# Kernel optimization log

Measured on AMD Instinct MI355X. Metric: run time of the kernel, lower is better.

Reference implementation:

```python
import jax, jax.numpy as jnp
import numpy as np

N_NODES = 10000
N_EDGES = 160000
N_GRAPHS = 64
X_IN = 128
HID = 64
EDGE_DIM = 16
HEADS = 4
# (in_dim, out_dim_per_head) for the 3 TransformerConv layers (concat=False)
DIMS = [(X_IN, HID), (HID, 2 * HID), (2 * HID, HID)]
WNAMES = [f"{n}{l}" for l in (1, 2, 3) for n in ("wq", "bq", "wk", "bk", "wv", "bv", "we", "ws", "bs")]


def setup_inputs() -> dict:
    key = jax.random.key(0)
    ks = iter(jax.random.split(key, 64))
    inp = {}
    inp["x"] = jax.random.normal(next(ks), (N_NODES, X_IN), jnp.float32)
    inp["edge_index"] = jax.random.randint(next(ks), (2, N_EDGES), 0, N_NODES)
    inp["edge_attr"] = jax.random.normal(next(ks), (N_EDGES, EDGE_DIM), jnp.float32)
    inp["batch"] = jnp.sort(jax.random.randint(next(ks), (N_NODES,), 0, N_GRAPHS))
    for l, (din, dout) in enumerate(DIMS, 1):
        hd = HEADS * dout
        for nm, shape in [("wq", (din, hd)), ("wk", (din, hd)), ("wv", (din, hd)),
                          ("we", (EDGE_DIM, hd)), ("ws", (din, dout))]:
            inp[f"{nm}{l}"] = jax.random.normal(next(ks), shape, jnp.float32) * 0.05
        inp[f"bq{l}"] = jnp.zeros((hd,), jnp.float32)
        inp[f"bk{l}"] = jnp.zeros((hd,), jnp.float32)
        inp[f"bv{l}"] = jnp.zeros((hd,), jnp.float32)
        inp[f"bs{l}"] = jnp.zeros((dout,), jnp.float32)
    return inp


def _transformer_conv(x, src, dst, edge_attr, wq, bq, wk, bk, wv, bv, we, ws, bs, dout):
    """PyG TransformerConv, concat=False, root_weight=True, with edge features."""
    N = x.shape[0]
    q = (x @ wq + bq).reshape(N, HEADS, dout)
    k = (x @ wk + bk).reshape(N, HEADS, dout)
    v = (x @ wv + bv).reshape(N, HEADS, dout)
    e = (edge_attr @ we).reshape(-1, HEADS, dout)  # [E, H, C]
    k_j = k[src] + e                               # edge-conditioned keys
    alpha = jnp.einsum("ehd,ehd->eh", q[dst], k_j) * (1.0 / float(dout) ** 0.5)  # [E, H]
    # numerically stable segment softmax over incoming edges of each dst node
    a_max = jax.ops.segment_max(alpha, dst, num_segments=N)
    ex = jnp.exp(alpha - a_max[dst])
    den = jax.ops.segment_sum(ex, dst, num_segments=N)
    attn = ex / den[dst]
    agg = jax.ops.segment_sum((v[src] + e) * attn[..., None], dst, num_segments=N)  # [N, H, C]
    return agg.mean(axis=1) + x @ ws + bs  # concat=False -> head mean; + skip


def _forward(x, edge_attr, edge_index, batch, params):
    src, dst = edge_index[0], edge_index[1]
    h = x
    for l, (_, dout) in enumerate(DIMS, 1):
        p = [params[f"{n}{l}"] for n in ("wq", "bq", "wk", "bk", "wv", "bv", "we", "ws", "bs")]
        h = jax.nn.elu(_transformer_conv(h, src, dst, edge_attr, *p, dout))
    # global mean pool over graphs
    s = jax.ops.segment_sum(h, batch, num_segments=N_GRAPHS)
    cnt = jax.ops.segment_sum(jnp.ones((h.shape[0], 1), h.dtype), batch, num_segments=N_GRAPHS)
    return s / jnp.maximum(cnt, 1.0)


def reference(x, edge_index, edge_attr, batch,
              wq1, bq1, wk1, bk1, wv1, bv1, we1, ws1, bs1,
              wq2, bq2, wk2, bk2, wv2, bv2, we2, ws2, bs2,
              wq3, bq3, wk3, bk3, wv3, bv3, we3, ws3, bs3):
    params = dict(locals())
    return _forward(x, edge_attr, edge_index, batch, params)
```

## Files before the change

kernel.cpp:

```cpp
#include <hip/hip_runtime.h>
#include <hip/hip_fp16.h>
#include <math.h>

#define N_NODES 10000
#define N_EDGES 160000
#define N_GRAPHS 64

using half8 = __attribute__((ext_vector_type(8))) _Float16;
using floatx4 = __attribute__((ext_vector_type(4))) float;

template <int NV> struct KW;
template <> struct KW<1> { using T = uint2; };
template <> struct KW<2> { using T = uint4; };

__device__ inline void cvt_kv(const uint2& w, float4* dst) {
  float2 a = __half22float2(*reinterpret_cast<const __half2*>(&w.x));
  float2 b = __half22float2(*reinterpret_cast<const __half2*>(&w.y));
  dst[0] = make_float4(a.x, a.y, b.x, b.y);
}
__device__ inline void cvt_kv(const uint4& w, float4* dst) {
  float2 a = __half22float2(*reinterpret_cast<const __half2*>(&w.x));
  float2 b = __half22float2(*reinterpret_cast<const __half2*>(&w.y));
  float2 c = __half22float2(*reinterpret_cast<const __half2*>(&w.z));
  float2 d = __half22float2(*reinterpret_cast<const __half2*>(&w.w));
  dst[0] = make_float4(a.x, a.y, b.x, b.y);
  dst[1] = make_float4(c.x, c.y, d.x, d.y);
}

template <int K, int HD, int DOUT>
__global__ __launch_bounds__(256) void gemm_mfma(
    const __half* __restrict__ A, const __half* __restrict__ Wp,
    const float* __restrict__ bias, __half* __restrict__ QS,
    __half* __restrict__ KV, int M) {
  constexpr int QSS = HD + 64 + DOUT;
  constexpr int KS = K / 32;
  const int tid = threadIdx.x;
  const int wave = tid >> 6, lane = tid & 63;
  const int quad = lane >> 4, n16 = lane & 15;
  const int row0 = blockIdx.y * 64 + wave * 16;
  const int col0 = blockIdx.x * 64;
  const int nblk0 = blockIdx.x * 4;

  const int arow = min(row0 + n16, M - 1);
  half8 afrag[KS];
#pragma unroll
  for (int s = 0; s < KS; ++s)
    afrag[s] = *reinterpret_cast<const half8*>(A + (size_t)arow * K + s * 32 + quad * 8);

  floatx4 acc[4];
#pragma unroll
  for (int t = 0; t < 4; ++t) {
    acc[t] = (floatx4){0.f, 0.f, 0.f, 0.f};
#pragma unroll
    for (int s = 0; s < KS; ++s) {
      half8 bf = *reinterpret_cast<const half8*>(
          Wp + (((size_t)(nblk0 + t) * KS + s) * 64 + lane) * 8);
      acc[t] = __builtin_amdgcn_mfma_f32_16x16x32_f16(afrag[s], bf, acc[t], 0, 0, 0);
    }
  }

#pragma unroll
  for (int t = 0; t < 4; ++t) {
    const int c = col0 + t * 16 + n16;
    const float bv = bias[c];
#pragma unroll
    for (int r = 0; r < 4; ++r) {
      int row = row0 + quad * 4 + r;
      if (row < M) {
        __half val = __float2half(acc[t][r] + bv);
        if (c < HD + 64)
          QS[(size_t)row * QSS + c] = val;
        else if (c < 3 * HD + 64)
          KV[(size_t)row * (2 * HD) + (c - HD - 64)] = val;
        else
          QS[(size_t)row * QSS + HD + 64 + (c - 3 * HD - 64)] = val;
      }
    }
  }
}

__device__ inline void pack_layer(int i, int K, int HD, int DOUT, float scale,
                                  const float* wq, const float* wk,
                                  const float* wv, const float* wsk,
                                  const float* we, const float* bq,
                                  const float* bk, const float* bv,
                                  const float* bs, __half* Wp, float* bcat) {
  const int W = 3 * HD + DOUT + 64;
  const int KS = K / 32;
  if (i < K * W) {
    int j = i & 7, lane = (i >> 3) & 63, fs = i >> 9;
    int nblk = fs / KS, s = fs - nblk * KS;
    int quad = lane >> 4, n = lane & 15;
    int k = s * 32 + quad * 8 + j, c = nblk * 16 + n;
    float v;
    if (c < HD) {
      v = wq[k * HD + c] * scale;
    } else if (c < HD + 64) {
      int gi = c - HD, hh = gi >> 4, d = gi & 15;
      float a = 0.f;
      for (int cc = 0; cc < DOUT; ++cc)
        a += wq[k * HD + hh * DOUT + cc] * we[d * HD + hh * DOUT + cc];
      v = a * scale;
    } else if (c < 2 * HD + 64) {
      v = wk[k * HD + (c - HD - 64)];
    } else if (c < 3 * HD + 64) {
      v = wv[k * HD + (c - 2 * HD - 64)];
    } else {
      v = wsk[k * DOUT + (c - 3 * HD - 64)];
    }
    Wp[i] = __float2half(v);
  } else {
    int c = i - K * W;
    float v;
    if (c < HD) {
      v = bq[c] * scale;
    } else if (c < HD + 64) {
      int gi = c - HD, hh = gi >> 4, d = gi & 15;
      float a = 0.f;
      for (int cc = 0; cc < DOUT; ++cc)
        a += bq[hh * DOUT + cc] * we[d * HD + hh * DOUT + cc];
      v = a * scale;
    } else if (c < 2 * HD + 64) {
      v = bk[c - HD - 64];
    } else if (c < 3 * HD + 64) {
      v = bv[c - 2 * HD - 64];
    } else {
      v = bs[c - 3 * HD - 64];
    }
    bcat[c] = v;
  }
}

#define T1 115584
#define T2 227904
#define T3 343488
#define TCONV (N_NODES * 32)
#define TTOT (T3 + TCONV)

__global__ void pack_all(
    const float* wq1, const float* wk1, const float* wv1, const float* ws1,
    const float* we1, const float* bq1, const float* bk1, const float* bv1,
    const float* bs1,
    const float* wq2, const float* wk2, const float* wv2, const float* ws2,
    const float* we2, const float* bq2, const float* bk2, const float* bv2,
    const float* bs2,
    const float* wq3, const float* wk3, const float* wv3, const float* ws3,
    const float* we3, const float* bq3, const float* bk3, const float* bv3,
    const float* bs3,
    __half* W1, float* b1, __half* W2, float* b2, __half* W3, float* b3,
    const float* x, __half* x16) {
  const float SC1 = 0.125f, SC2 = 0.08838834764831845f;
  for (int i = blockIdx.x * blockDim.x + threadIdx.x; i < TTOT;
       i += gridDim.x * blockDim.x) {
    if (i < T1)
      pack_layer(i, 128, 256, 64, SC1, wq1, wk1, wv1, ws1, we1, bq1, bk1, bv1, bs1, W1, b1);
    else if (i < T2)
      pack_layer(i - T1, 64, 512, 128, SC2, wq2, wk2, wv2, ws2, we2, bq2, bk2, bv2, bs2, W2, b2);
    else if (i < T3)
      pack_layer(i - T2, 128, 256, 64, SC1, wq3, wk3, wv3, ws3, we3, bq3, bk3, bv3, bs3, W3, b3);
    else {
      int k = i - T3;
      float4 v = reinterpret_cast<const float4*>(x)[k];
      __half2* o = reinterpret_cast<__half2*>(x16) + 2 * k;
      o[0] = __floats2half2_rn(v.x, v.y);
      o[1] = __floats2half2_rn(v.z, v.w);
    }
  }
}

__global__ void count_dst(const int* __restrict__ dst, int* __restrict__ cnt) {
  int e = blockIdx.x * blockDim.x + threadIdx.x;
  if (e < N_EDGES) atomicAdd(&cnt[dst[e]], 1);
}

__global__ __launch_bounds__(256) void scan_offs(const int* __restrict__ cnt,
                                                 int* __restrict__ offs) {
  __shared__ int part[256];
  const int t = threadIdx.x;
  const int chunk = (N_NODES + 255) / 256;
  const int b = t * chunk;
  const int e = min(N_NODES, b + chunk);
  int s = 0;
  for (int i = b; i < e; ++i) s += cnt[i];
  part[t] = s;
  __syncthreads();
  for (int off = 1; off < 256; off <<= 1) {
    int v = (t >= off) ? part[t - off] : 0;
    __syncthreads();
    part[t] += v;
    __syncthreads();
  }
  int pre = (t == 0) ? 0 : part[t - 1];
  for (int i = b; i < e; ++i) { offs[i] = pre; pre += cnt[i]; }
  if (t == 0) offs[N_NODES] = part[255];
}

__global__ void scatter_csr(const int* __restrict__ src, const int* __restrict__ dst,
                            const float* __restrict__ edge_attr,
                            const int* __restrict__ offs, int* __restrict__ cursor,
                            int* __restrict__ csr_src, float* __restrict__ csr_ea) {
  int e = blockIdx.x * blockDim.x + threadIdx.x;
  if (e < N_EDGES) {
    int d = dst[e];
    int pos = offs[d] + atomicAdd(&cursor[d], 1);
    csr_src[pos] = src[e];
    float4* o4 = reinterpret_cast<float4*>(csr_ea + (size_t)pos * 16);
    const float4* s4 = reinterpret_cast<const float4*>(edge_attr + (size_t)e * 16);
    o4[0] = s4[0]; o4[1] = s4[1]; o4[2] = s4[2]; o4[3] = s4[3];
  }
}

template <int DOUT>
__global__ __launch_bounds__(256) void edge_attn(
    const __half* __restrict__ QS, const __half* __restrict__ KV,
    const float* __restrict__ we, const int* __restrict__ csr_src,
    const float* __restrict__ csr_ea, const int* __restrict__ offs,
    float* __restrict__ out, __half* __restrict__ out16) {
  constexpr int HD = 4 * DOUT;
  constexpr int QSS = HD + 64 + DOUT;
  constexpr int KVS = 2 * HD;
  constexpr int NV = DOUT / 64;
  using KWT = typename KW<NV>::T;

  const int lane = threadIdx.x & 63;
  const int h = lane >> 4, t16 = lane & 15;
  const int n = blockIdx.x * 4 + (threadIdx.x >> 6);
  const int c0 = t16 * 4 * NV;

  const __half* base = QS + (size_t)n * QSS;
  float4 q[NV], acc[NV];
  {
    KWT qw = *reinterpret_cast<const KWT*>(base + h * DOUT + c0);
    cvt_kv(qw, q);
  }
#pragma unroll
  for (int v = 0; v < NV; ++v) acc[v] = make_float4(0.f, 0.f, 0.f, 0.f);
  const float g = __half2float(base[HD + h * 16 + t16]);

  float lsum = 0.f, tacc = 0.f;

  const int s0 = offs[n], s1 = offs[n + 1];

  int sjA[4], sjB[4];
  float eaA[4], eaB[4];
  KWT krA[4], vrA[4], krB[4], vrB[4];

  auto load_grp = [&](int bi, int (&sj)[4], float (&ea)[4], KWT (&kr)[4],
                      KWT (&vr)[4]) {
#pragma unroll
    for (int j = 0; j < 4; ++j) sj[j] = csr_src[bi + j];
#pragma unroll
    for (int j = 0; j < 4; ++j) ea[j] = csr_ea[(size_t)(bi + j) * 16 + t16];
#pragma unroll
    for (int j = 0; j < 4; ++j) {
      const __half* rb = KV + (size_t)sj[j] * KVS + h * DOUT + c0;
      kr[j] = *reinterpret_cast<const KWT*>(rb);
      vr[j] = *reinterpret_cast<const KWT*>(rb + HD);
    }
  };

  auto compute_grp = [&](float (&ea)[4], KWT (&kr)[4], KWT (&vr)[4]) {
    float a[4];
#pragma unroll
    for (int j = 0; j < 4; ++j) {
      float4 kk[NV];
      cvt_kv(kr[j], kk);
      float p = ea[j] * g;
#pragma unroll
      for (int v = 0; v < NV; ++v)
        p += q[v].x * kk[v].x + q[v].y * kk[v].y + q[v].z * kk[v].z +
             q[v].w * kk[v].w;
      a[j] = p;
    }
#pragma unroll
    for (int j = 0; j < 4; ++j) {
      a[j] += __shfl_xor(a[j], 1);
      a[j] += __shfl_xor(a[j], 2);
      a[j] += __shfl_xor(a[j], 4);
      a[j] += __shfl_xor(a[j], 8);
    }
    float p0 = __expf(a[0]), p1 = __expf(a[1]);
    float p2 = __expf(a[2]), p3 = __expf(a[3]);
    lsum += p0 + p1 + p2 + p3;
    tacc += p0 * ea[0] + p1 * ea[1] + p2 * ea[2] + p3 * ea[3];
    float pj[4] = {p0, p1, p2, p3};
#pragma unroll
    for (int j = 0; j < 4; ++j) {
      float4 vv[NV];
      cvt_kv(vr[j], vv);
#pragma unroll
      for (int v = 0; v < NV; ++v) {
        acc[v].x += pj[j] * vv[v].x;
        acc[v].y += pj[j] * vv[v].y;
        acc[v].z += pj[j] * vv[v].z;
        acc[v].w += pj[j] * vv[v].w;
      }
    }
  };

  int ii = s0;
  const int end_full = s0 + ((s1 - s0) & ~3);
  if (ii < end_full) {
    load_grp(ii, sjA, eaA, krA, vrA);
    for (;;) {
      if (ii + 4 >= end_full) { compute_grp(eaA, krA, vrA); ii += 4; break; }
      load_grp(ii + 4, sjB, eaB, krB, vrB);
      compute_grp(eaA, krA, vrA);
      ii += 4;
      if (ii + 4 >= end_full) { compute_grp(eaB, krB, vrB); ii += 4; break; }
      load_grp(ii + 4, sjA, eaA, krA, vrA);
      compute_grp(eaB, krB, vrB);
      ii += 4;
    }
  }

  for (; ii < s1; ++ii) {
    int s = csr_src[ii];
    float ea0 = csr_ea[(size_t)ii * 16 + t16];
    const __half* rb = KV + (size_t)s * KVS + h * DOUT + c0;
    KWT kw = *reinterpret_cast<const KWT*>(rb);
    KWT vw = *reinterpret_cast<const KWT*>(rb + HD);
    float4 kk[NV], vv[NV];
    cvt_kv(kw, kk);
    cvt_kv(vw, vv);
    float a = ea0 * g;
#pragma unroll
    for (int v = 0; v < NV; ++v)
      a += q[v].x * kk[v].x + q[v].y * kk[v].y + q[v].z * kk[v].z + q[v].w * kk[v].w;
    a += __shfl_xor(a, 1);
    a += __shfl_xor(a, 2);
    a += __shfl_xor(a, 4);
    a += __shfl_xor(a, 8);
    float p = __expf(a);
    lsum += p;
    tacc += p * ea0;
#pragma unroll
    for (int v = 0; v < NV; ++v) {
      acc[v].x += p * vv[v].x;
      acc[v].y += p * vv[v].y;
      acc[v].z += p * vv[v].z;
      acc[v].w += p * vv[v].w;
    }
  }

  float invl = (lsum > 0.f) ? 1.f / lsum : 0.f;
  float tn = tacc * invl;
  float4 val[NV];
#pragma unroll
  for (int v = 0; v < NV; ++v) {
    val[v].x = acc[v].x * invl; val[v].y = acc[v].y * invl;
    val[v].z = acc[v].z * invl; val[v].w = acc[v].w * invl;
  }
#pragma unroll
  for (int d = 0; d < 16; ++d) {
    float td = __shfl(tn, (lane & 48) | d);
    const float* wb = we + d * HD + h * DOUT + c0;
#pragma unroll
    for (int v = 0; v < NV; ++v) {
      float4 w4 = *reinterpret_cast<const float4*>(wb + 4 * v);
      val[v].x += td * w4.x; val[v].y += td * w4.y;
      val[v].z += td * w4.z; val[v].w += td * w4.w;
    }
  }
#pragma unroll
  for (int v = 0; v < NV; ++v) {
    val[v].x += __shfl_xor(val[v].x, 16); val[v].x += __shfl_xor(val[v].x, 32);
    val[v].y += __shfl_xor(val[v].y, 16); val[v].y += __shfl_xor(val[v].y, 32);
    val[v].z += __shfl_xor(val[v].z, 16); val[v].z += __shfl_xor(val[v].z, 32);
    val[v].w += __shfl_xor(val[v].w, 16); val[v].w += __shfl_xor(val[v].w, 32);
  }
  if (h == 0) {
    KWT sw = *reinterpret_cast<const KWT*>(base + HD + 64 + c0);
    float4 sk[NV];
    cvt_kv(sw, sk);
#pragma unroll
    for (int v = 0; v < NV; ++v) {
      float4 o;
      o.x = 0.25f * val[v].x + sk[v].x;
      o.y = 0.25f * val[v].y + sk[v].y;
      o.z = 0.25f * val[v].z + sk[v].z;
      o.w = 0.25f * val[v].w + sk[v].w;
      o.x = (o.x > 0.f) ? o.x : expm1f(o.x);
      o.y = (o.y > 0.f) ? o.y : expm1f(o.y);
      o.z = (o.z > 0.f) ? o.z : expm1f(o.z);
      o.w = (o.w > 0.f) ? o.w : expm1f(o.w);
      *reinterpret_cast<float4*>(out + (size_t)n * DOUT + c0 + 4 * v) = o;
      __half2* o16 = reinterpret_cast<__half2*>(out16 + (size_t)n * DOUT + c0 + 4 * v);
      o16[0] = __floats2half2_rn(o.x, o.y);
      o16[1] = __floats2half2_rn(o.z, o.w);
    }
  }
}

__device__ inline int lower_bound(const int* b, int n, int v) {
  int lo = 0, hi = n;
  while (lo < hi) {
    int mid = (lo + hi) >> 1;
    if (b[mid] < v) lo = mid + 1; else hi = mid;
  }
  return lo;
}

__global__ __launch_bounds__(256) void pool_all(const float* __restrict__ h,
                                                const int* __restrict__ batch,
                                                float* __restrict__ out) {
  const int g = blockIdx.x;
  const int start = lower_bound(batch, N_NODES, g);
  const int end = lower_bound(batch, N_NODES, g + 1);
  const int c = threadIdx.x & 63, j = threadIdx.x >> 6;
  float s = 0.f;
  for (int n = start + j; n < end; n += 4) s += h[(size_t)n * 64 + c];
  __shared__ float red[4][64];
  red[j][c] = s;
  __syncthreads();
  if (j == 0) {
    float tot = red[0][c] + red[1][c] + red[2][c] + red[3][c];
    out[g * 64 + c] = tot / (float)max(end - start, 1);
  }
}

extern "C" void kernel_launch(void* const* d_in, const int* in_sizes, int n_in,
                              void* d_out, int out_size, void* d_ws, size_t ws_size,
                              hipStream_t stream) {
  const float* x = (const float*)d_in[0];
  const int* edge_index = (const int*)d_in[1];
  const float* edge_attr = (const float*)d_in[2];
  const int* batch = (const int*)d_in[3];
  const int* srcp = edge_index;
  const int* dstp = edge_index + N_EDGES;

  const bool dict_order = in_sizes[5] > 1024;
  const float *wq[3], *wk[3], *wv[3], *wep[3], *wsk[3], *bq[3], *bk[3], *bv[3], *bs[3];
  for (int L = 0; L < 3; ++L) {
    int b = 4 + L * 9;
    if (dict_order) {
      wq[L] = (const float*)d_in[b + 0];
      wk[L] = (const float*)d_in[b + 1];
      wv[L] = (const float*)d_in[b + 2];
      wep[L] = (const float*)d_in[b + 3];
      wsk[L] = (const float*)d_in[b + 4];
      bq[L] = (const float*)d_in[b + 5];
      bk[L] = (const float*)d_in[b + 6];
      bv[L] = (const float*)d_in[b + 7];
      bs[L] = (const float*)d_in[b + 8];
    } else {
      wq[L] = (const float*)d_in[b + 0];
      bq[L] = (const float*)d_in[b + 1];
      wk[L] = (const float*)d_in[b + 2];
      bk[L] = (const float*)d_in[b + 3];
      wv[L] = (const float*)d_in[b + 4];
      bv[L] = (const float*)d_in[b + 5];
      wep[L] = (const float*)d_in[b + 6];
      wsk[L] = (const float*)d_in[b + 7];
      bs[L] = (const float*)d_in[b + 8];
    }
  }

  char* p = (char*)d_ws;
  __half* qs = (__half*)p;    p += (size_t)N_NODES * 704 * 2;
  __half* kv = (__half*)p;    p += (size_t)N_NODES * 1024 * 2;
  float* h1 = (float*)p;      p += (size_t)N_NODES * 64 * 4;
  float* h2 = (float*)p;      p += (size_t)N_NODES * 128 * 4;
  __half* x16 = (__half*)p;   p += (size_t)N_NODES * 128 * 2;
  __half* h16 = (__half*)p;   p += (size_t)N_NODES * 128 * 2;
  __half* W1 = (__half*)p;    p += 128 * 896 * 2;
  __half* W2 = (__half*)p;    p += 64 * 1728 * 2;
  __half* W3 = (__half*)p;    p += 128 * 896 * 2;
  float* b1 = (float*)p;      p += 896 * 4;
  float* b2 = (float*)p;      p += 1728 * 4;
  float* b3 = (float*)p;      p += 896 * 4;
  float* csr_ea = (float*)p;  p += (size_t)N_EDGES * 16 * 4;
  int* cnt = (int*)p;         p += N_NODES * 4;
  int* cursor = (int*)p;      p += N_NODES * 4;
  int* offs = (int*)p;        p += (N_NODES + 1) * 4;
  int* csr_src = (int*)p;     p += N_EDGES * 4;

  pack_all<<<1024, 256, 0, stream>>>(
      wq[0], wk[0], wv[0], wsk[0], wep[0], bq[0], bk[0], bv[0], bs[0],
      wq[1], wk[1], wv[1], wsk[1], wep[1], bq[1], bk[1], bv[1], bs[1],
      wq[2], wk[2], wv[2], wsk[2], wep[2], bq[2], bk[2], bv[2], bs[2],
      W1, b1, W2, b2, W3, b3, x, x16);

  hipMemsetAsync(cnt, 0, 2 * N_NODES * sizeof(int), stream);
  count_dst<<<(N_EDGES + 255) / 256, 256, 0, stream>>>(dstp, cnt);
  scan_offs<<<1, 256, 0, stream>>>(cnt, offs);
  scatter_csr<<<(N_EDGES + 255) / 256, 256, 0, stream>>>(srcp, dstp, edge_attr,
                                                         offs, cursor, csr_src, csr_ea);

  const int MT = (N_NODES + 63) / 64;
  gemm_mfma<128, 256, 64><<<dim3(896 / 64, MT), 256, 0, stream>>>(x16, W1, b1, qs,
                                                                  kv, N_NODES);
  edge_attn<64><<<N_NODES / 4, 256, 0, stream>>>(qs, kv, wep[0], csr_src, csr_ea,
                                                 offs, h1, h16);
  gemm_mfma<64, 512, 128><<<dim3(1728 / 64, MT), 256, 0, stream>>>(h16, W2, b2, qs,
                                                                   kv, N_NODES);
  edge_attn<128><<<N_NODES / 4, 256, 0, stream>>>(qs, kv, wep[1], csr_src, csr_ea,
                                                  offs, h2, h16);
  gemm_mfma<128, 256, 64><<<dim3(896 / 64, MT), 256, 0, stream>>>(h16, W3, b3, qs,
                                                                  kv, N_NODES);
  edge_attn<64><<<N_NODES / 4, 256, 0, stream>>>(qs, kv, wep[2], csr_src, csr_ea,
                                                 offs, h1, x16 );

  pool_all<<<N_GRAPHS, 256, 0, stream>>>(h1, batch, (float*)d_out);
}
```

Before: 354.0 us.

## Split edge attention across two waves per node and interleave K/V rows

The edge attention kernel now gives each destination node two waves. Each wave takes alternating groups of four edges, and the partial softmax sums and value accumulators are merged through shared memory, which doubles parallelism per node and the number of loads in flight. The GEMM epilogue stages its tile in LDS and writes vectorized rows, storing K and V interleaved per lane so that one gather load fetches both. The CSR scan also moves to 1024 threads. In exchange the kernel adds shared memory, a block barrier and a merge step, and the second wave sits idle during the tail edges.

```diff
diff --git a/kernel.cpp b/kernel.cpp
--- a/kernel.cpp
+++ b/kernel.cpp
@@ -27,21 +27,34 @@
   dst[1] = make_float4(c.x, c.y, d.x, d.y);
 }
 
+__device__ inline void load_kv_pair(const __half* rb, uint2& kr, uint2& vr) {
+  uint4 w = *reinterpret_cast<const uint4*>(rb);
+  kr = make_uint2(w.x, w.y);
+  vr = make_uint2(w.z, w.w);
+}
+__device__ inline void load_kv_pair(const __half* rb, uint4& kr, uint4& vr) {
+  kr = *reinterpret_cast<const uint4*>(rb);
+  vr = *reinterpret_cast<const uint4*>(rb + 8);
+}
+
 template <int K, int HD, int DOUT>
 __global__ __launch_bounds__(256) void gemm_mfma(
     const __half* __restrict__ A, const __half* __restrict__ Wp,
     const float* __restrict__ bias, __half* __restrict__ QS,
     __half* __restrict__ KV, int M) {
   constexpr int QSS = HD + 64 + DOUT;
+  constexpr int KVS = 2 * HD;
+  constexpr int NV = DOUT / 64;
   constexpr int KS = K / 32;
+  __shared__ __half st[64][72];
   const int tid = threadIdx.x;
   const int wave = tid >> 6, lane = tid & 63;
   const int quad = lane >> 4, n16 = lane & 15;
-  const int row0 = blockIdx.y * 64 + wave * 16;
+  const int row0 = blockIdx.y * 64;
   const int col0 = blockIdx.x * 64;
   const int nblk0 = blockIdx.x * 4;
 
-  const int arow = min(row0 + n16, M - 1);
+  const int arow = min(row0 + wave * 16 + n16, M - 1);
   half8 afrag[KS];
 #pragma unroll
   for (int s = 0; s < KS; ++s)
@@ -61,20 +74,40 @@
 
 #pragma unroll
   for (int t = 0; t < 4; ++t) {
-    const int c = col0 + t * 16 + n16;
-    const float bv = bias[c];
-#pragma unroll
-    for (int r = 0; r < 4; ++r) {
-      int row = row0 + quad * 4 + r;
-      if (row < M) {
-        __half val = __float2half(acc[t][r] + bv);
-        if (c < HD + 64)
-          QS[(size_t)row * QSS + c] = val;
-        else if (c < 3 * HD + 64)
-          KV[(size_t)row * (2 * HD) + (c - HD - 64)] = val;
-        else
-          QS[(size_t)row * QSS + HD + 64 + (c - 3 * HD - 64)] = val;
-      }
+    float bv = bias[col0 + t * 16 + n16];
+#pragma unroll
+    for (int r = 0; r < 4; ++r)
+      st[wave * 16 + quad * 4 + r][t * 16 + n16] = __float2half(acc[t][r] + bv);
+  }
+  __syncthreads();
+
+  if (col0 < HD + 64 || col0 >= 3 * HD + 64) {
+    const int qcol = (col0 < HD + 64) ? col0 : (HD + 64 + (col0 - 3 * HD - 64));
+    for (int c = tid; c < 512; c += 256) {
+      int r = c >> 3, seg = c & 7;
+      int row = row0 + r;
+      if (row < M)
+        *reinterpret_cast<uint4*>(QS + (size_t)row * QSS + qcol + seg * 8) =
+            *reinterpret_cast<const uint4*>(&st[r][seg * 8]);
+    }
+  } else {
+    constexpr int G = 4 * NV;
+    constexpr int NG = 64 / G;
+    const int ckv0 = col0 - (HD + 64);
+    for (int c = tid; c < 64 * NG; c += 256) {
+      int r = c / NG, gl = c % NG;
+      int row = row0 + r;
+      if (row >= M) continue;
+      int ckv = ckv0 + gl * G;
+      int off;
+      if (ckv < HD) off = (ckv / G) * (2 * G);
+      else          off = ((ckv - HD) / G) * (2 * G) + G;
+      if (NV == 1)
+        *reinterpret_cast<uint2*>(KV + (size_t)row * KVS + off) =
+            *reinterpret_cast<const uint2*>(&st[r][gl * G]);
+      else
+        *reinterpret_cast<uint4*>(KV + (size_t)row * KVS + off) =
+            *reinterpret_cast<const uint4*>(&st[r][gl * G]);
     }
   }
 }
@@ -173,18 +206,18 @@
   if (e < N_EDGES) atomicAdd(&cnt[dst[e]], 1);
 }
 
-__global__ __launch_bounds__(256) void scan_offs(const int* __restrict__ cnt,
-                                                 int* __restrict__ offs) {
-  __shared__ int part[256];
+__global__ __launch_bounds__(1024) void scan_offs(const int* __restrict__ cnt,
+                                                  int* __restrict__ offs) {
+  __shared__ int part[1024];
   const int t = threadIdx.x;
-  const int chunk = (N_NODES + 255) / 256;
+  const int chunk = (N_NODES + 1023) / 1024;
   const int b = t * chunk;
   const int e = min(N_NODES, b + chunk);
   int s = 0;
   for (int i = b; i < e; ++i) s += cnt[i];
   part[t] = s;
   __syncthreads();
-  for (int off = 1; off < 256; off <<= 1) {
+  for (int off = 1; off < 1024; off <<= 1) {
     int v = (t >= off) ? part[t - off] : 0;
     __syncthreads();
     part[t] += v;
@@ -192,7 +225,7 @@
   }
   int pre = (t == 0) ? 0 : part[t - 1];
   for (int i = b; i < e; ++i) { offs[i] = pre; pre += cnt[i]; }
-  if (t == 0) offs[N_NODES] = part[255];
+  if (t == 0) offs[N_NODES] = part[1023];
 }
 
 __global__ void scatter_csr(const int* __restrict__ src, const int* __restrict__ dst,
@@ -222,10 +255,16 @@
   constexpr int NV = DOUT / 64;
   using KWT = typename KW<NV>::T;
 
+  __shared__ float sacc[2][HD];
+  __shared__ float sl[2][64], stc[2][64];
+
   const int lane = threadIdx.x & 63;
+  const int wid = threadIdx.x >> 6;
+  const int nl = wid >> 1, half = wid & 1;
   const int h = lane >> 4, t16 = lane & 15;
-  const int n = blockIdx.x * 4 + (threadIdx.x >> 6);
+  const int n = blockIdx.x * 2 + nl;
   const int c0 = t16 * 4 * NV;
+  const int bofs = (h * 16 + t16) * 8 * NV;
 
   const __half* base = QS + (size_t)n * QSS;
   float4 q[NV], acc[NV];
@@ -240,6 +279,7 @@
   float lsum = 0.f, tacc = 0.f;
 
   const int s0 = offs[n], s1 = offs[n + 1];
+  const int end_full = s0 + ((s1 - s0) & ~3);
 
   int sjA[4], sjB[4];
   float eaA[4], eaB[4];
@@ -252,11 +292,8 @@
 #pragma unroll
     for (int j = 0; j < 4; ++j) ea[j] = csr_ea[(size_t)(bi + j) * 16 + t16];
 #pragma unroll
-    for (int j = 0; j < 4; ++j) {
-      const __half* rb = KV + (size_t)sj[j] * KVS + h * DOUT + c0;
-      kr[j] = *reinterpret_cast<const KWT*>(rb);
-      vr[j] = *reinterpret_cast<const KWT*>(rb + HD);
-    }
+    for (int j = 0; j < 4; ++j)
+      load_kv_pair(KV + (size_t)sj[j] * KVS + bofs, kr[j], vr[j]);
   };
 
   auto compute_grp = [&](float (&ea)[4], KWT (&kr)[4], KWT (&vr)[4]) {
@@ -298,49 +335,76 @@
     }
   };
 
-  int ii = s0;
-  const int end_full = s0 + ((s1 - s0) & ~3);
+  int ii = s0 + half * 4;
   if (ii < end_full) {
     load_grp(ii, sjA, eaA, krA, vrA);
     for (;;) {
-      if (ii + 4 >= end_full) { compute_grp(eaA, krA, vrA); ii += 4; break; }
-      load_grp(ii + 4, sjB, eaB, krB, vrB);
+      int nx = ii + 8;
+      if (nx >= end_full) { compute_grp(eaA, krA, vrA); break; }
+      load_grp(nx, sjB, eaB, krB, vrB);
       compute_grp(eaA, krA, vrA);
-      ii += 4;
-      if (ii + 4 >= end_full) { compute_grp(eaB, krB, vrB); ii += 4; break; }
-      load_grp(ii + 4, sjA, eaA, krA, vrA);
+      ii = nx; nx = ii + 8;
+      if (nx >= end_full) { compute_grp(eaB, krB, vrB); break; }
+      load_grp(nx, sjA, eaA, krA, vrA);
       compute_grp(eaB, krB, vrB);
-      ii += 4;
-    }
-  }
-
-  for (; ii < s1; ++ii) {
-    int s = csr_src[ii];
-    float ea0 = csr_ea[(size_t)ii * 16 + t16];
-    const __half* rb = KV + (size_t)s * KVS + h * DOUT + c0;
-    KWT kw = *reinterpret_cast<const KWT*>(rb);
-    KWT vw = *reinterpret_cast<const KWT*>(rb + HD);
-    float4 kk[NV], vv[NV];
-    cvt_kv(kw, kk);
-    cvt_kv(vw, vv);
-    float a = ea0 * g;
-#pragma unroll
-    for (int v = 0; v < NV; ++v)
-      a += q[v].x * kk[v].x + q[v].y * kk[v].y + q[v].z * kk[v].z + q[v].w * kk[v].w;
-    a += __shfl_xor(a, 1);
-    a += __shfl_xor(a, 2);
-    a += __shfl_xor(a, 4);
-    a += __shfl_xor(a, 8);
-    float p = __expf(a);
-    lsum += p;
-    tacc += p * ea0;
+      ii = nx;
+    }
+  }
+
+  if (half == 0) {
+    for (int t = end_full; t < s1; ++t) {
+      int s = csr_src[t];
+      float ea0 = csr_ea[(size_t)t * 16 + t16];
+      KWT kw, vw;
+      load_kv_pair(KV + (size_t)s * KVS + bofs, kw, vw);
+      float4 kk[NV], vv[NV];
+      cvt_kv(kw, kk);
+      cvt_kv(vw, vv);
+      float a = ea0 * g;
+#pragma unroll
+      for (int v = 0; v < NV; ++v)
+        a += q[v].x * kk[v].x + q[v].y * kk[v].y + q[v].z * kk[v].z + q[v].w * kk[v].w;
+      a += __shfl_xor(a, 1);
+      a += __shfl_xor(a, 2);
+      a += __shfl_xor(a, 4);
+      a += __shfl_xor(a, 8);
+      float p = __expf(a);
+      lsum += p;
+      tacc += p * ea0;
+#pragma unroll
+      for (int v = 0; v < NV; ++v) {
+        acc[v].x += p * vv[v].x;
+        acc[v].y += p * vv[v].y;
+        acc[v].z += p * vv[v].z;
+        acc[v].w += p * vv[v].w;
+      }
+    }
+  }
+
+  if (half == 1) {
 #pragma unroll
     for (int v = 0; v < NV; ++v) {
-      acc[v].x += p * vv[v].x;
-      acc[v].y += p * vv[v].y;
-      acc[v].z += p * vv[v].z;
-      acc[v].w += p * vv[v].w;
-    }
+      int cb = h * DOUT + c0 + 4 * v;
+      sacc[nl][cb + 0] = acc[v].x;
+      sacc[nl][cb + 1] = acc[v].y;
+      sacc[nl][cb + 2] = acc[v].z;
+      sacc[nl][cb + 3] = acc[v].w;
+    }
+    sl[nl][lane] = lsum;
+    stc[nl][lane] = tacc;
+  }
+  __syncthreads();
+  if (half != 0) return;
+
+  lsum += sl[nl][lane];
+  tacc += stc[nl][lane];
+#pragma unroll
+  for (int v = 0; v < NV; ++v) {
+    int cb = h * DOUT + c0 + 4 * v;
+    acc[v].x += sacc[nl][cb + 0];
+    acc[v].y += sacc[nl][cb + 1];
+    acc[v].z += sacc[nl][cb + 2];
+    acc[v].w += sacc[nl][cb + 3];
   }
 
   float invl = (lsum > 0.f) ? 1.f / lsum : 0.f;
@@ -483,22 +547,22 @@
 
   hipMemsetAsync(cnt, 0, 2 * N_NODES * sizeof(int), stream);
   count_dst<<<(N_EDGES + 255) / 256, 256, 0, stream>>>(dstp, cnt);
-  scan_offs<<<1, 256, 0, stream>>>(cnt, offs);
+  scan_offs<<<1, 1024, 0, stream>>>(cnt, offs);
   scatter_csr<<<(N_EDGES + 255) / 256, 256, 0, stream>>>(srcp, dstp, edge_attr,
                                                          offs, cursor, csr_src, csr_ea);
 
   const int MT = (N_NODES + 63) / 64;
   gemm_mfma<128, 256, 64><<<dim3(896 / 64, MT), 256, 0, stream>>>(x16, W1, b1, qs,
                                                                   kv, N_NODES);
-  edge_attn<64><<<N_NODES / 4, 256, 0, stream>>>(qs, kv, wep[0], csr_src, csr_ea,
+  edge_attn<64><<<N_NODES / 2, 256, 0, stream>>>(qs, kv, wep[0], csr_src, csr_ea,
                                                  offs, h1, h16);
   gemm_mfma<64, 512, 128><<<dim3(1728 / 64, MT), 256, 0, stream>>>(h16, W2, b2, qs,
                                                                    kv, N_NODES);
-  edge_attn<128><<<N_NODES / 4, 256, 0, stream>>>(qs, kv, wep[1], csr_src, csr_ea,
+  edge_attn<128><<<N_NODES / 2, 256, 0, stream>>>(qs, kv, wep[1], csr_src, csr_ea,
                                                   offs, h2, h16);
   gemm_mfma<128, 256, 64><<<dim3(896 / 64, MT), 256, 0, stream>>>(h16, W3, b3, qs,
                                                                   kv, N_NODES);
-  edge_attn<64><<<N_NODES / 4, 256, 0, stream>>>(qs, kv, wep[2], csr_src, csr_ea,
+  edge_attn<64><<<N_NODES / 2, 256, 0, stream>>>(qs, kv, wep[2], csr_src, csr_ea,
                                                  offs, h1, x16 );
 
   pool_all<<<N_GRAPHS, 256, 0, stream>>>(h1, batch, (float*)d_out);
```

New measurement: 374.3 us. +5.7%, slower.

## Sort nodes by in-degree for edge attention scheduling and skip unused fp32 stores

Applied to the files above, without the earlier changes.

The scan kernel now builds a degree histogram and a permutation that orders nodes by descending in-degree (counting sort, capped at 255). Each edge_attn block then processes nodes in that order, so waves in a block get similar edge counts, less lane idling, and the heaviest nodes start first. The fp32 output store is also skipped for the first two layers, which only need the fp16 copy. The single-block scan grows to 1024 threads and adds shared-memory atomics, and scattered node indices weaken output write locality.

```diff
diff --git a/kernel.cpp b/kernel.cpp
--- a/kernel.cpp
+++ b/kernel.cpp
@@ -173,26 +173,46 @@
   if (e < N_EDGES) atomicAdd(&cnt[dst[e]], 1);
 }
 
-__global__ __launch_bounds__(256) void scan_offs(const int* __restrict__ cnt,
-                                                 int* __restrict__ offs) {
-  __shared__ int part[256];
+__global__ __launch_bounds__(1024) void scan_offs(const int* __restrict__ cnt,
+                                                  int* __restrict__ offs,
+                                                  int* __restrict__ perm) {
+  __shared__ int part[1024];
+  __shared__ int hist[256], hstart[256], hcur[256];
   const int t = threadIdx.x;
-  const int chunk = (N_NODES + 255) / 256;
+  const int chunk = (N_NODES + 1023) / 1024;
   const int b = t * chunk;
   const int e = min(N_NODES, b + chunk);
+  if (t < 256) { hist[t] = 0; hcur[t] = 0; }
+  __syncthreads();
   int s = 0;
-  for (int i = b; i < e; ++i) s += cnt[i];
+  for (int i = b; i < e; ++i) {
+    int d = cnt[i];
+    s += d;
+    atomicAdd(&hist[min(d, 255)], 1);
+  }
   part[t] = s;
   __syncthreads();
-  for (int off = 1; off < 256; off <<= 1) {
+  for (int off = 1; off < 1024; off <<= 1) {
     int v = (t >= off) ? part[t - off] : 0;
     __syncthreads();
     part[t] += v;
     __syncthreads();
   }
+  if (t == 0) {
+    int acc = 0;
+    for (int bk = 255; bk >= 0; --bk) { hstart[bk] = acc; acc += hist[bk]; }
+    offs[N_NODES] = part[1023];
+  }
+  __syncthreads();
   int pre = (t == 0) ? 0 : part[t - 1];
-  for (int i = b; i < e; ++i) { offs[i] = pre; pre += cnt[i]; }
-  if (t == 0) offs[N_NODES] = part[255];
+  for (int i = b; i < e; ++i) {
+    offs[i] = pre;
+    int d = cnt[i];
+    pre += d;
+    int bkt = min(d, 255);
+    int pos = hstart[bkt] + atomicAdd(&hcur[bkt], 1);
+    perm[pos] = i;
+  }
 }
 
 __global__ void scatter_csr(const int* __restrict__ src, const int* __restrict__ dst,
@@ -210,12 +230,13 @@
   }
 }
 
-template <int DOUT>
+template <int DOUT, bool W32>
 __global__ __launch_bounds__(256) void edge_attn(
     const __half* __restrict__ QS, const __half* __restrict__ KV,
     const float* __restrict__ we, const int* __restrict__ csr_src,
     const float* __restrict__ csr_ea, const int* __restrict__ offs,
-    float* __restrict__ out, __half* __restrict__ out16) {
+    const int* __restrict__ perm, float* __restrict__ out,
+    __half* __restrict__ out16) {
   constexpr int HD = 4 * DOUT;
   constexpr int QSS = HD + 64 + DOUT;
   constexpr int KVS = 2 * HD;
@@ -224,7 +245,7 @@
 
   const int lane = threadIdx.x & 63;
   const int h = lane >> 4, t16 = lane & 15;
-  const int n = blockIdx.x * 4 + (threadIdx.x >> 6);
+  const int n = perm[blockIdx.x * 4 + (threadIdx.x >> 6)];
   const int c0 = t16 * 4 * NV;
 
   const __half* base = QS + (size_t)n * QSS;
@@ -303,14 +324,15 @@
   if (ii < end_full) {
     load_grp(ii, sjA, eaA, krA, vrA);
     for (;;) {
-      if (ii + 4 >= end_full) { compute_grp(eaA, krA, vrA); ii += 4; break; }
-      load_grp(ii + 4, sjB, eaB, krB, vrB);
+      int nx = ii + 4;
+      if (nx >= end_full) { compute_grp(eaA, krA, vrA); ii = nx; break; }
+      load_grp(nx, sjB, eaB, krB, vrB);
       compute_grp(eaA, krA, vrA);
-      ii += 4;
-      if (ii + 4 >= end_full) { compute_grp(eaB, krB, vrB); ii += 4; break; }
-      load_grp(ii + 4, sjA, eaA, krA, vrA);
+      ii = nx; nx = ii + 4;
+      if (nx >= end_full) { compute_grp(eaB, krB, vrB); ii = nx; break; }
+      load_grp(nx, sjA, eaA, krA, vrA);
       compute_grp(eaB, krB, vrB);
-      ii += 4;
+      ii = nx;
     }
   }
 
@@ -384,7 +406,8 @@
       o.y = (o.y > 0.f) ? o.y : expm1f(o.y);
       o.z = (o.z > 0.f) ? o.z : expm1f(o.z);
       o.w = (o.w > 0.f) ? o.w : expm1f(o.w);
-      *reinterpret_cast<float4*>(out + (size_t)n * DOUT + c0 + 4 * v) = o;
+      if (W32)
+        *reinterpret_cast<float4*>(out + (size_t)n * DOUT + c0 + 4 * v) = o;
       __half2* o16 = reinterpret_cast<__half2*>(out16 + (size_t)n * DOUT + c0 + 4 * v);
       o16[0] = __floats2half2_rn(o.x, o.y);
       o16[1] = __floats2half2_rn(o.z, o.w);
@@ -460,7 +483,6 @@
   __half* qs = (__half*)p;    p += (size_t)N_NODES * 704 * 2;
   __half* kv = (__half*)p;    p += (size_t)N_NODES * 1024 * 2;
   float* h1 = (float*)p;      p += (size_t)N_NODES * 64 * 4;
-  float* h2 = (float*)p;      p += (size_t)N_NODES * 128 * 4;
   __half* x16 = (__half*)p;   p += (size_t)N_NODES * 128 * 2;
   __half* h16 = (__half*)p;   p += (size_t)N_NODES * 128 * 2;
   __half* W1 = (__half*)p;    p += 128 * 896 * 2;
@@ -473,6 +495,7 @@
   int* cnt = (int*)p;         p += N_NODES * 4;
   int* cursor = (int*)p;      p += N_NODES * 4;
   int* offs = (int*)p;        p += (N_NODES + 1) * 4;
+  int* perm = (int*)p;        p += N_NODES * 4;
   int* csr_src = (int*)p;     p += N_EDGES * 4;
 
   pack_all<<<1024, 256, 0, stream>>>(
@@ -483,23 +506,23 @@
 
   hipMemsetAsync(cnt, 0, 2 * N_NODES * sizeof(int), stream);
   count_dst<<<(N_EDGES + 255) / 256, 256, 0, stream>>>(dstp, cnt);
-  scan_offs<<<1, 256, 0, stream>>>(cnt, offs);
+  scan_offs<<<1, 1024, 0, stream>>>(cnt, offs, perm);
   scatter_csr<<<(N_EDGES + 255) / 256, 256, 0, stream>>>(srcp, dstp, edge_attr,
                                                          offs, cursor, csr_src, csr_ea);
 
   const int MT = (N_NODES + 63) / 64;
   gemm_mfma<128, 256, 64><<<dim3(896 / 64, MT), 256, 0, stream>>>(x16, W1, b1, qs,
                                                                   kv, N_NODES);
-  edge_attn<64><<<N_NODES / 4, 256, 0, stream>>>(qs, kv, wep[0], csr_src, csr_ea,
-                                                 offs, h1, h16);
+  edge_attn<64, false><<<N_NODES / 4, 256, 0, stream>>>(qs, kv, wep[0], csr_src,
+                                                        csr_ea, offs, perm, h1, h16);
   gemm_mfma<64, 512, 128><<<dim3(1728 / 64, MT), 256, 0, stream>>>(h16, W2, b2, qs,
                                                                    kv, N_NODES);
-  edge_attn<128><<<N_NODES / 4, 256, 0, stream>>>(qs, kv, wep[1], csr_src, csr_ea,
-                                                  offs, h2, h16);
+  edge_attn<128, false><<<N_NODES / 4, 256, 0, stream>>>(qs, kv, wep[1], csr_src,
+                                                         csr_ea, offs, perm, h1, h16);
   gemm_mfma<128, 256, 64><<<dim3(896 / 64, MT), 256, 0, stream>>>(h16, W3, b3, qs,
                                                                   kv, N_NODES);
-  edge_attn<64><<<N_NODES / 4, 256, 0, stream>>>(qs, kv, wep[2], csr_src, csr_ea,
-                                                 offs, h1, x16 );
+  edge_attn<64, true><<<N_NODES / 4, 256, 0, stream>>>(qs, kv, wep[2], csr_src,
+                                                       csr_ea, offs, perm, h1, x16);
 
   pool_all<<<N_GRAPHS, 256, 0, stream>>>(h1, batch, (float*)d_out);
 }
```

Result: no change. 356.7 us (+0.8%).
